# Optimization experiments

Hardware: AMD Instinct MI355X
Metric: run time of the kernel (lower is better)

## Reference

```python
import jax, jax.numpy as jnp
import numpy as np

D_MODEL = 1024
D_STATE = 32
EXPAND = 2
D_INNER = D_MODEL * EXPAND          # 2048
DT_RANK = D_MODEL // 16             # 64
LN_EPS = 1e-5


def setup_inputs() -> dict:
    key = jax.random.key(0)
    ks = jax.random.split(key, 9)
    s = 0.02
    x = jax.random.normal(ks[0], (2, 2048, D_MODEL), dtype=jnp.float32)
    W_in = jax.random.normal(ks[1], (2 * D_INNER, D_MODEL), dtype=jnp.float32) * s
    W_x = jax.random.normal(ks[2], (DT_RANK + 2 * D_STATE, D_INNER), dtype=jnp.float32) * s
    W_dt = jax.random.normal(ks[3], (D_INNER, DT_RANK), dtype=jnp.float32) * s
    b_dt = jax.random.normal(ks[4], (D_INNER,), dtype=jnp.float32) * s
    A_real0 = jax.random.normal(ks[5], (D_INNER, D_STATE), dtype=jnp.float32) * 0.5
    A_log_real = jnp.log(jnp.clip(-A_real0, 1e-4, None))
    A_imag = jax.random.normal(ks[6], (D_INNER, D_STATE), dtype=jnp.float32) * 0.1
    D_param = jnp.ones((D_INNER,), dtype=jnp.float32)
    W_out = jax.random.normal(ks[7], (D_MODEL, D_INNER), dtype=jnp.float32) * s
    ln_g = jnp.ones((D_MODEL,), dtype=jnp.float32)
    ln_b = jnp.zeros((D_MODEL,), dtype=jnp.float32)
    return {"x": x, "W_in": W_in, "W_x": W_x, "W_dt": W_dt, "b_dt": b_dt,
            "A_log_real": A_log_real, "A_imag": A_imag, "D_param": D_param,
            "W_out": W_out, "ln_g": ln_g, "ln_b": ln_b}


def _forward(x, W_in, W_x, W_dt, b_dt, A_log_real, A_imag, D_param, W_out, ln_g, ln_b):
    B, T, _ = x.shape
    residual = x
    # LayerNorm
    mu = jnp.mean(x, axis=-1, keepdims=True)
    var = jnp.mean((x - mu) ** 2, axis=-1, keepdims=True)
    xn = (x - mu) * jax.lax.rsqrt(var + LN_EPS) * ln_g + ln_b
    # in_proj -> (x_ssm, z)
    xz = jnp.einsum('btd,ed->bte', xn, W_in)            # (B,T,2*d_inner)
    x_ssm, z = jnp.split(xz, 2, axis=-1)
    # x_proj -> dt_low, B, C
    x_dbl = jnp.einsum('bte,re->btr', x_ssm, W_x)        # (B,T,dt_rank+2*d_state)
    dt_low = x_dbl[..., :DT_RANK]
    B_param = x_dbl[..., DT_RANK:DT_RANK + D_STATE]      # (B,T,N)
    C_param = x_dbl[..., DT_RANK + D_STATE:]             # (B,T,N)
    dt = jax.nn.softplus(jnp.einsum('btr,er->bte', dt_low, W_dt) + b_dt)  # (B,T,d_inner)
    # A = -exp(A_log_real) + i * A_imag, complex state split into (hr, hi)
    Ar = -jnp.exp(A_log_real)                             # (d_inner,N)
    Ai = A_imag

    def step(carry, inp):
        hr, hi = carry                                    # (B,d_inner,N)
        dt_t, B_t, C_t, x_t = inp                         # (B,d_inner),(B,N),(B,N),(B,d_inner)
        dtE = dt_t[:, :, None]                            # (B,d_inner,1)
        scale = jnp.exp(Ar[None] * dtE)
        ang = Ai[None] * dtE
        dAr = scale * jnp.cos(ang)
        dAi = scale * jnp.sin(ang)
        dBx = (dt_t * x_t)[:, :, None] * B_t[:, None, :]  # real input injection
        hr2 = dAr * hr - dAi * hi + dBx
        hi2 = dAr * hi + dAi * hr
        y = jnp.sum(hr2 * C_t[:, None, :], axis=-1)       # real part of (h * C).sum
        return (hr2, hi2), y

    h0 = jnp.zeros((B, D_INNER, D_STATE), dtype=x.dtype)
    xs = (jnp.transpose(dt, (1, 0, 2)), jnp.transpose(B_param, (1, 0, 2)),
          jnp.transpose(C_param, (1, 0, 2)), jnp.transpose(x_ssm, (1, 0, 2)))
    _, ys = jax.lax.scan(step, (h0, h0), xs)              # (T,B,d_inner)
    y = jnp.transpose(ys, (1, 0, 2)) + D_param * x_ssm
    y = y * jax.nn.silu(z)
    out = jnp.einsum('bte,de->btd', y, W_out)
    return residual + out  # dropout is identity at eval


def reference(x, W_in, W_x, W_dt, b_dt, A_log_real, A_imag, D_param, W_out, ln_g, ln_b):
    return _forward(x, W_in, W_x, W_dt, b_dt, A_log_real, A_imag, D_param, W_out, ln_g, ln_b)
```

## Files before the change

### kernel.cpp

```cpp
#include <hip/hip_runtime.h>
#include <math.h>

#define D_MODEL 1024
#define D_STATE 32
#define D_INNER 2048
#define DT_RANK 64
#define BT 4096
#define XZLD 4224
#define LN_EPS 1e-5f

typedef __attribute__((ext_vector_type(8))) short short8;
typedef __attribute__((ext_vector_type(4))) float f32x4;
typedef const __attribute__((address_space(1))) void* gp_t;
typedef __attribute__((address_space(3))) void* lp_t;

__device__ __forceinline__ ushort bf16r(float f) {
    unsigned u = __float_as_uint(f);
    u += 0x7fff + ((u >> 16) & 1);
    return (ushort)(u >> 16);
}

__device__ __forceinline__ float dpp_red16(float x) {
    int t;
    t = __builtin_amdgcn_update_dpp(0, __float_as_int(x), 0x111, 0xf, 0xf, true);
    x += __int_as_float(t);
    t = __builtin_amdgcn_update_dpp(0, __float_as_int(x), 0x112, 0xf, 0xf, true);
    x += __int_as_float(t);
    t = __builtin_amdgcn_update_dpp(0, __float_as_int(x), 0x114, 0xf, 0xf, true);
    x += __int_as_float(t);
    t = __builtin_amdgcn_update_dpp(0, __float_as_int(x), 0x118, 0xf, 0xf, true);
    x += __int_as_float(t);
    return x;
}

__global__ __launch_bounds__(256) void prep_weights(
    const float* __restrict__ W_in, const float* __restrict__ W_out,
    const float* __restrict__ W_dt, const float* __restrict__ W_x,
    ushort* __restrict__ Waug, ushort* __restrict__ Wout_bf,
    ushort* __restrict__ Wdt_bf, ushort* __restrict__ Wx_bf) {
    int bid = blockIdx.x;
    const float* src; ushort* dst; int i;
    if (bid < 4096)      { src = W_in;  dst = Waug;    i = bid * 256 + threadIdx.x; }
    else if (bid < 6144) { src = W_out; dst = Wout_bf; i = (bid - 4096) * 256 + threadIdx.x; }
    else if (bid < 6400) { src = W_x;   dst = Wx_bf;   i = (bid - 6144) * 256 + threadIdx.x; }
    else                 { src = W_dt;  dst = Wdt_bf;  i = (bid - 6400) * 256 + threadIdx.x; }
    float4 v = ((const float4*)src)[i];
    ushort4 o;
    o.x = bf16r(v.x); o.y = bf16r(v.y); o.z = bf16r(v.z); o.w = bf16r(v.w);
    ((ushort4*)dst)[i] = o;
}

__global__ __launch_bounds__(256) void cvt_dtlow(const float* __restrict__ xz,
                                                 ushort* __restrict__ out) {
    int i = blockIdx.x * 256 + threadIdx.x;
    int row = i >> 4, c = (i & 15) << 2;
    float4 v = *(const float4*)&xz[(size_t)row * XZLD + 4096 + c];
    ushort4 o;
    o.x = bf16r(v.x); o.y = bf16r(v.y); o.z = bf16r(v.z); o.w = bf16r(v.w);
    ((ushort4*)out)[i] = o;
}

__global__ __launch_bounds__(256) void transpose_cvt(const float* __restrict__ in,
                                                     ushort* __restrict__ out) {
    __shared__ float tile[32][33];
    int bx = blockIdx.x * 32;
    int by = blockIdx.y * 32;
    int tx = threadIdx.x & 31, ty = threadIdx.x >> 5;
    #pragma unroll
    for (int i = 0; i < 32; i += 8)
        tile[ty + i][tx] = in[(size_t)(bx + ty + i) * 1024 + by + tx];
    __syncthreads();
    #pragma unroll
    for (int i = 0; i < 32; i += 8)
        out[(size_t)(by + ty + i) * 2048 + bx + tx] = bf16r(tile[tx][ty + i]);
}

__global__ __launch_bounds__(256) void ln_kernel(const float* __restrict__ x,
                                                 const float* __restrict__ g,
                                                 const float* __restrict__ b,
                                                 ushort* __restrict__ xn) {
    int row = blockIdx.x;
    const float4* xr = (const float4*)(x + (size_t)row * D_MODEL);
    float4 v = xr[threadIdx.x];
    float s  = v.x + v.y + v.z + v.w;
    float ss = v.x*v.x + v.y*v.y + v.z*v.z + v.w*v.w;
    #pragma unroll
    for (int off = 32; off > 0; off >>= 1) {
        s  += __shfl_down(s,  off, 64);
        ss += __shfl_down(ss, off, 64);
    }
    __shared__ float rs[4], rss[4];
    int wave = threadIdx.x >> 6;
    if ((threadIdx.x & 63) == 0) { rs[wave] = s; rss[wave] = ss; }
    __syncthreads();
    s  = rs[0] + rs[1] + rs[2] + rs[3];
    ss = rss[0] + rss[1] + rss[2] + rss[3];
    float mu  = s * (1.f / D_MODEL);
    float var = ss * (1.f / D_MODEL) - mu * mu;
    float inv = rsqrtf(var + LN_EPS);
    float4 gv = ((const float4*)g)[threadIdx.x];
    float4 bv = ((const float4*)b)[threadIdx.x];
    ushort4 o;
    o.x = bf16r((v.x - mu) * inv * gv.x + bv.x);
    o.y = bf16r((v.y - mu) * inv * gv.y + bv.y);
    o.z = bf16r((v.z - mu) * inv * gv.z + bv.z);
    o.w = bf16r((v.w - mu) * inv * gv.w + bv.w);
    ((ushort4*)(xn + (size_t)row * D_MODEL))[threadIdx.x] = o;
}

template<int RESID, int ACT, int OBF>
__global__ __launch_bounds__(256) void gemm_bt_bf16(
    const ushort* __restrict__ A, const ushort* __restrict__ B,
    void* __restrict__ Cv, int ldc, int K,
    const float* __restrict__ resid, const float* __restrict__ bias)
{
    __shared__ __align__(16) ushort As[128 * 32];
    __shared__ __align__(16) ushort Bs[128 * 32];
    int tid = threadIdx.x;
    int bm = blockIdx.x * 128, bn = blockIdx.y * 128;
    int wave = tid >> 6, lane = tid & 63;
    int wm = (wave & 1) * 64, wn = (wave >> 1) * 64;
    int quad = lane >> 4, m16 = lane & 15;
    int grow = tid >> 2;
    int gcol = (tid & 3) * 8;
    const size_t a0 = (size_t)(bm + grow) * K + gcol;
    const size_t b0 = (size_t)(bn + grow) * K + gcol;
    char* asw = (char*)As + wave * 1024;
    char* bsw = (char*)Bs + wave * 1024;

    f32x4 acc[4][4] = {};
    for (int k0 = 0; k0 < K; k0 += 32) {
        __builtin_amdgcn_global_load_lds((gp_t)(A + a0 + k0),                 (lp_t)asw,          16, 0, 0);
        __builtin_amdgcn_global_load_lds((gp_t)(A + a0 + (size_t)64*K + k0),  (lp_t)(asw + 4096), 16, 0, 0);
        __builtin_amdgcn_global_load_lds((gp_t)(B + b0 + k0),                 (lp_t)bsw,          16, 0, 0);
        __builtin_amdgcn_global_load_lds((gp_t)(B + b0 + (size_t)64*K + k0),  (lp_t)(bsw + 4096), 16, 0, 0);
        __syncthreads();
        short8 af[4], bf[4];
        #pragma unroll
        for (int i = 0; i < 4; ++i)
            af[i] = *(const short8*)&As[(wm + i * 16 + m16) * 32 + quad * 8];
        #pragma unroll
        for (int j = 0; j < 4; ++j)
            bf[j] = *(const short8*)&Bs[(wn + j * 16 + m16) * 32 + quad * 8];
        #pragma unroll
        for (int i = 0; i < 4; ++i)
            #pragma unroll
            for (int j = 0; j < 4; ++j)
                acc[i][j] = __builtin_amdgcn_mfma_f32_16x16x32_bf16(
                    af[i], bf[j], acc[i][j], 0, 0, 0);
        __syncthreads();
    }
    #pragma unroll
    for (int i = 0; i < 4; ++i) {
        #pragma unroll
        for (int r = 0; r < 4; ++r) {
            int row = bm + wm + i * 16 + quad * 4 + r;
            #pragma unroll
            for (int j = 0; j < 4; ++j) {
                int col = bn + wn + j * 16 + m16;
                float v = acc[i][j][r];
                if (ACT == 1) {
                    v += bias[col];
                    v = (v > 20.f) ? v : __logf(1.f + __expf(v));
                }
                if (RESID) v += resid[(size_t)row * ldc + col];
                if (OBF) ((ushort*)Cv)[(size_t)row * ldc + col] = bf16r(v);
                else     ((float*) Cv)[(size_t)row * ldc + col] = v;
            }
        }
    }
}

__global__ __launch_bounds__(256) void scan_kernel(
    const float* __restrict__ xz,
    const float* __restrict__ dtm,
    const float* __restrict__ A_log_real,
    const float* __restrict__ A_imag,
    const float* __restrict__ D_param,
    ushort* __restrict__ y)
{
    const int tid  = threadIdx.x;
    const int lane = tid & 63;
    const int s    = tid & 31;
    const int elb  = tid >> 5;
    const int b    = blockIdx.x >> 8;
    const int e0   = (blockIdx.x & 255) << 3;
    const int e    = e0 + elb;
    const int stt  = tid >> 3, sk  = tid & 7;
    const int btp  = tid >> 4, bsp = tid & 15;
    const int q    = (lane >> 4) & 1;

    __shared__ __align__(16) float dxp[2][8][17][4];
    __shared__ __align__(16) float xzs[2][8][34][2];
    __shared__ __align__(16) float bcs[2][16][33][4];
    __shared__ __align__(16) float pp[8][2][32];

    const float Ar2  = -__expf(A_log_real[e * D_STATE + s]) * 1.44269504f;
    const float Ai2p = A_imag[e * D_STATE + s] * 0.15915494f;
    const float Dps  = D_param[e0 + sk];
    float hr = 0.f, hi = 0.f;
    const float* xzb = xz + (size_t)b * 2048 * XZLD;
    const float* bcb = xzb + 4096 + DT_RANK;
    const float* dtb = dtm + (size_t)b * 2048 * 2048;
    ushort*      yb  = y   + (size_t)b * 2048 * 2048;

    float r_d, r_x, r_z;
    float2 rB0, rC0, rB1, rC1;

#define LOADC(T0) do {                                                        \
    r_d = dtb[(size_t)((T0) + stt) * 2048 + e0 + sk];                         \
    r_x = xzb[(size_t)((T0) + stt) * XZLD + e0 + sk];                         \
    r_z = xzb[(size_t)((T0) + stt) * XZLD + 2048 + e0 + sk];                  \
    rB0 = *(const float2*)&bcb[(size_t)((T0) + 2*btp) * XZLD + 2*bsp];        \
    rC0 = *(const float2*)&bcb[(size_t)((T0) + 2*btp) * XZLD + 32 + 2*bsp];   \
    rB1 = *(const float2*)&bcb[(size_t)((T0) + 2*btp+1) * XZLD + 2*bsp];      \
    rC1 = *(const float2*)&bcb[(size_t)((T0) + 2*btp+1) * XZLD + 32 + 2*bsp]; \
  } while (0)

#define STAGE(NB) do {                                                        \
    float dtx = r_d * r_x;                                                    \
    float gg  = r_z / (1.f + __expf(-r_z));                                   \
    float Dx  = Dps * r_x;                                                    \
    *(float2*)&dxp[NB][sk][stt >> 1][(stt & 1) * 2] = make_float2(r_d, dtx);  \
    *(float2*)&xzs[NB][sk][stt] = make_float2(Dx, gg);                        \
    *(float4*)&bcs[NB][btp][2*bsp][0]   = make_float4(rB0.x, rC0.x, rB1.x, rC1.x); \
    *(float4*)&bcs[NB][btp][2*bsp+1][0] = make_float4(rB0.y, rC0.y, rB1.y, rC1.y); \
  } while (0)

    LOADC(0);
    STAGE(0);
    for (int c = 0; c < 64; ++c) {
        const int buf = c & 1;
        __syncthreads();
        if (c < 63) LOADC((c + 1) * 32);
        #pragma unroll
        for (int tp = 0; tp < 16; ++tp) {
            float4 dd = *(const float4*)&dxp[buf][elb][tp][0];
            float4 bc = *(const float4*)&bcs[buf][tp][s][0];
            float sc = __builtin_amdgcn_exp2f(Ar2 * dd.x);
            float u  = Ai2p * dd.x;
            float sa = __builtin_amdgcn_sinf(u), ca = __builtin_amdgcn_cosf(u);
            float dAr = sc * ca, dAi = sc * sa;
            float hrn = fmaf(dAr, hr, fmaf(-dAi, hi, dd.y * bc.x));
            hi = fmaf(dAr, hi, dAi * hr); hr = hrn;
            float p0 = hr * bc.y;
            sc = __builtin_amdgcn_exp2f(Ar2 * dd.z);
            u  = Ai2p * dd.z;
            sa = __builtin_amdgcn_sinf(u); ca = __builtin_amdgcn_cosf(u);
            dAr = sc * ca; dAi = sc * sa;
            hrn = fmaf(dAr, hr, fmaf(-dAi, hi, dd.w * bc.z));
            hi = fmaf(dAr, hi, dAi * hr); hr = hrn;
            float p1 = hr * bc.w;
            p0 = dpp_red16(p0);
            p1 = dpp_red16(p1);
            if ((lane & 15) == 15)
                *(float2*)&pp[elb][q][2 * tp] = make_float2(p0, p1);
        }
        float pA = pp[elb][0][s];
        float pB = pp[elb][1][s];
        float2 xg = *(const float2*)&xzs[buf][elb][s];
        yb[(size_t)(c * 32 + s) * 2048 + e] = bf16r((pA + pB + xg.x) * xg.y);
        if (c < 63) STAGE(buf ^ 1);
    }
#undef LOADC
#undef STAGE
}

extern "C" void kernel_launch(void* const* d_in, const int* in_sizes, int n_in,
                              void* d_out, int out_size, void* d_ws, size_t ws_size,
                              hipStream_t stream) {
    const float* x          = (const float*)d_in[0];
    const float* W_in       = (const float*)d_in[1];
    const float* W_x        = (const float*)d_in[2];
    const float* W_dt       = (const float*)d_in[3];
    const float* b_dt       = (const float*)d_in[4];
    const float* A_log_real = (const float*)d_in[5];
    const float* A_imag     = (const float*)d_in[6];
    const float* D_param    = (const float*)d_in[7];
    const float* W_out      = (const float*)d_in[8];
    const float* ln_g       = (const float*)d_in[9];
    const float* ln_b       = (const float*)d_in[10];
    float* out = (float*)d_out;

    char* ws = (char*)d_ws;
    float*  xz       = (float*) (ws);
    float*  dt       = (float*) (ws + ((size_t) 66 << 20));
    ushort* xn_bf    = (ushort*)(ws + ((size_t) 98 << 20));
    ushort* Waug     = (ushort*)(ws + ((size_t)106 << 20));
    ushort* y_bf     = (ushort*)(ws + ((size_t)115 << 20));
    ushort* Wout_bf  = (ushort*)(ws + ((size_t)131 << 20));
    ushort* Wdt_bf   = (ushort*)(ws + ((size_t)135 << 20));
    ushort* dtlow_bf = (ushort*)(ws + ((size_t)136 << 20));
    ushort* Wx_bf   = (ushort*)(ws + ((size_t)  1 << 20));
    ushort* WinT_bf = (ushort*)(ws + ((size_t)  2 << 20));

    prep_weights<<<6528, 256, 0, stream>>>(W_in, W_out, W_dt, W_x,
                                           Waug, Wout_bf, Wdt_bf, Wx_bf);
    transpose_cvt<<<dim3(64, 32), 256, 0, stream>>>(W_in, WinT_bf);
    gemm_bt_bf16<0,0,1><<<dim3(1, 8), 256, 0, stream>>>(
        Wx_bf, WinT_bf, Waug + (size_t)4096 * 1024, 1024, 2048, nullptr, nullptr);
    ln_kernel<<<BT, 256, 0, stream>>>(x, ln_g, ln_b, xn_bf);
    gemm_bt_bf16<0,0,0><<<dim3(BT/128, XZLD/128), 256, 0, stream>>>(
        xn_bf, Waug, xz, XZLD, D_MODEL, nullptr, nullptr);
    cvt_dtlow<<<256, 256, 0, stream>>>(xz, dtlow_bf);
    gemm_bt_bf16<0,1,0><<<dim3(BT/128, D_INNER/128), 256, 0, stream>>>(
        dtlow_bf, Wdt_bf, dt, D_INNER, DT_RANK, nullptr, b_dt);
    scan_kernel<<<512, 256, 0, stream>>>(xz, dt, A_log_real, A_imag, D_param, y_bf);
    gemm_bt_bf16<1,0,0><<<dim3(BT/128, D_MODEL/128), 256, 0, stream>>>(
        y_bf, Wout_bf, out, D_MODEL, D_INNER, x, nullptr);
}
```

Measured before the change: 501.7 us.

## Repack SSM intermediates into scan-friendly bf16 layouts and fuse epilogues

The in_proj GEMM epilogue now writes x and silu(z) as packed bf16 pairs in a per-channel-group, time-major layout, and writes dt_low and B/C as bf16 directly, which removes the fp32 xz buffer and the separate dt_low conversion kernel. The dt GEMM writes softplus output in the same grouped layout, so the scan reads contiguous per-group data. The scan stages y through a small LDS tile and stores it in a packed layout that a new N=64-tile out_proj GEMM reads directly. The weight transpose is merged into the prep kernel. This lowers memory traffic and launch count, at the cost of scattered epilogue stores and more bf16 rounding of x, z, B and C.

```diff
diff --git a/kernel.cpp b/kernel.cpp
--- a/kernel.cpp
+++ b/kernel.cpp
@@ -6,7 +6,6 @@
 #define D_INNER 2048
 #define DT_RANK 64
 #define BT 4096
-#define XZLD 4224
 #define LN_EPS 1e-5f
 
 typedef __attribute__((ext_vector_type(8))) short short8;
@@ -19,6 +18,8 @@
     u += 0x7fff + ((u >> 16) & 1);
     return (ushort)(u >> 16);
 }
+__device__ __forceinline__ float bflo(unsigned u) { return __uint_as_float(u << 16); }
+__device__ __forceinline__ float bfhi(unsigned u) { return __uint_as_float(u & 0xffff0000u); }
 
 __device__ __forceinline__ float dpp_red16(float x) {
     int t;
@@ -37,42 +38,33 @@
     const float* __restrict__ W_in, const float* __restrict__ W_out,
     const float* __restrict__ W_dt, const float* __restrict__ W_x,
     ushort* __restrict__ Waug, ushort* __restrict__ Wout_bf,
-    ushort* __restrict__ Wdt_bf, ushort* __restrict__ Wx_bf) {
+    ushort* __restrict__ Wdt_bf, ushort* __restrict__ Wx_bf,
+    ushort* __restrict__ WinT_bf) {
+    __shared__ float tile[32][33];
     int bid = blockIdx.x;
-    const float* src; ushort* dst; int i;
-    if (bid < 4096)      { src = W_in;  dst = Waug;    i = bid * 256 + threadIdx.x; }
-    else if (bid < 6144) { src = W_out; dst = Wout_bf; i = (bid - 4096) * 256 + threadIdx.x; }
-    else if (bid < 6400) { src = W_x;   dst = Wx_bf;   i = (bid - 6144) * 256 + threadIdx.x; }
-    else                 { src = W_dt;  dst = Wdt_bf;  i = (bid - 6400) * 256 + threadIdx.x; }
-    float4 v = ((const float4*)src)[i];
-    ushort4 o;
-    o.x = bf16r(v.x); o.y = bf16r(v.y); o.z = bf16r(v.z); o.w = bf16r(v.w);
-    ((ushort4*)dst)[i] = o;
-}
-
-__global__ __launch_bounds__(256) void cvt_dtlow(const float* __restrict__ xz,
-                                                 ushort* __restrict__ out) {
-    int i = blockIdx.x * 256 + threadIdx.x;
-    int row = i >> 4, c = (i & 15) << 2;
-    float4 v = *(const float4*)&xz[(size_t)row * XZLD + 4096 + c];
-    ushort4 o;
-    o.x = bf16r(v.x); o.y = bf16r(v.y); o.z = bf16r(v.z); o.w = bf16r(v.w);
-    ((ushort4*)out)[i] = o;
-}
-
-__global__ __launch_bounds__(256) void transpose_cvt(const float* __restrict__ in,
-                                                     ushort* __restrict__ out) {
-    __shared__ float tile[32][33];
-    int bx = blockIdx.x * 32;
-    int by = blockIdx.y * 32;
-    int tx = threadIdx.x & 31, ty = threadIdx.x >> 5;
-    #pragma unroll
-    for (int i = 0; i < 32; i += 8)
-        tile[ty + i][tx] = in[(size_t)(bx + ty + i) * 1024 + by + tx];
-    __syncthreads();
-    #pragma unroll
-    for (int i = 0; i < 32; i += 8)
-        out[(size_t)(by + ty + i) * 2048 + bx + tx] = bf16r(tile[tx][ty + i]);
+    if (bid < 6528) {
+        const float* src; ushort* dst; int i;
+        if (bid < 4096)      { src = W_in;  dst = Waug;    i = bid * 256 + threadIdx.x; }
+        else if (bid < 6144) { src = W_out; dst = Wout_bf; i = (bid - 4096) * 256 + threadIdx.x; }
+        else if (bid < 6400) { src = W_x;   dst = Wx_bf;   i = (bid - 6144) * 256 + threadIdx.x; }
+        else                 { src = W_dt;  dst = Wdt_bf;  i = (bid - 6400) * 256 + threadIdx.x; }
+        float4 v = ((const float4*)src)[i];
+        ushort4 o;
+        o.x = bf16r(v.x); o.y = bf16r(v.y); o.z = bf16r(v.z); o.w = bf16r(v.w);
+        ((ushort4*)dst)[i] = o;
+    } else {
+        int bid2 = bid - 6528;
+        int bx = (bid2 & 63) * 32;
+        int by = (bid2 >> 6) * 32;
+        int tx = threadIdx.x & 31, ty = threadIdx.x >> 5;
+        #pragma unroll
+        for (int i = 0; i < 32; i += 8)
+            tile[ty + i][tx] = W_in[(size_t)(bx + ty + i) * 1024 + by + tx];
+        __syncthreads();
+        #pragma unroll
+        for (int i = 0; i < 32; i += 8)
+            WinT_bf[(size_t)(by + ty + i) * 2048 + bx + tx] = bf16r(tile[tx][ty + i]);
+    }
 }
 
 __global__ __launch_bounds__(256) void ln_kernel(const float* __restrict__ x,
@@ -108,11 +100,13 @@
     ((ushort4*)(xn + (size_t)row * D_MODEL))[threadIdx.x] = o;
 }
 
-template<int RESID, int ACT, int OBF>
+template<int MODE>
 __global__ __launch_bounds__(256) void gemm_bt_bf16(
     const ushort* __restrict__ A, const ushort* __restrict__ B,
-    void* __restrict__ Cv, int ldc, int K,
-    const float* __restrict__ resid, const float* __restrict__ bias)
+    float* __restrict__ C, int ldc, int K,
+    const float* __restrict__ resid, const float* __restrict__ bias,
+    ushort* __restrict__ xg16, ushort* __restrict__ dtlow_bf,
+    ushort* __restrict__ bc_bf, float* __restrict__ dtp)
 {
     __shared__ __align__(16) ushort As[128 * 32];
     __shared__ __align__(16) ushort Bs[128 * 32];
@@ -159,33 +153,107 @@
             for (int j = 0; j < 4; ++j) {
                 int col = bn + wn + j * 16 + m16;
                 float v = acc[i][j][r];
-                if (ACT == 1) {
+                if (MODE == 0) {
+                    C[(size_t)row * ldc + col] = v;
+                } else if (MODE == 1) {
+                    ((ushort*)C)[(size_t)row * ldc + col] = bf16r(v);
+                } else if (MODE == 2) {
+                    int bb = row >> 11, t = row & 2047;
+                    if (col < 2048) {
+                        size_t slot = ((size_t)(bb * 256 + (col >> 3)) * 2048 + t) * 8 + (col & 7);
+                        xg16[slot * 2] = bf16r(v);
+                    } else if (col < 4096) {
+                        int e2 = col - 2048;
+                        float gg = v / (1.f + __expf(-v));
+                        size_t slot = ((size_t)(bb * 256 + (e2 >> 3)) * 2048 + t) * 8 + (e2 & 7);
+                        xg16[slot * 2 + 1] = bf16r(gg);
+                    } else if (col < 4160) {
+                        dtlow_bf[(size_t)row * 64 + (col - 4096)] = bf16r(v);
+                    } else {
+                        bc_bf[(size_t)row * 64 + (col - 4160)] = bf16r(v);
+                    }
+                } else {
                     v += bias[col];
                     v = (v > 20.f) ? v : __logf(1.f + __expf(v));
+                    int bb = row >> 11, t = row & 2047;
+                    dtp[((size_t)(bb * 256 + (col >> 3)) * 2048 + t) * 8 + (col & 7)] = v;
                 }
-                if (RESID) v += resid[(size_t)row * ldc + col];
-                if (OBF) ((ushort*)Cv)[(size_t)row * ldc + col] = bf16r(v);
-                else     ((float*) Cv)[(size_t)row * ldc + col] = v;
             }
         }
     }
 }
 
+__global__ __launch_bounds__(256) void gemm4_n64(
+    const ushort* __restrict__ A, const ushort* __restrict__ B,
+    float* __restrict__ C, const float* __restrict__ resid)
+{
+    __shared__ __align__(16) ushort As[128 * 32];
+    __shared__ __align__(16) ushort Bs[64 * 32];
+    int tid = threadIdx.x;
+    int bm = blockIdx.x * 128, bn = blockIdx.y * 64;
+    int wave = tid >> 6, lane = tid & 63;
+    int wm = (wave & 1) * 64, wn = (wave >> 1) * 32;
+    int quad = lane >> 4, m16 = lane & 15;
+    int grow = tid >> 2;
+    int gcol = (tid & 3) * 8;
+    int bb = bm >> 11, t0 = bm & 2047;
+    const size_t b0 = (size_t)(bn + grow) * 2048 + gcol;
+    char* asw = (char*)As + wave * 1024;
+    char* bsw = (char*)Bs + wave * 1024;
+
+    f32x4 acc[4][2] = {};
+    for (int k0 = 0; k0 < 2048; k0 += 32) {
+        size_t abase = (size_t)(bb * 256 + ((k0 + gcol) >> 3)) * 2048;
+        __builtin_amdgcn_global_load_lds((gp_t)(A + (abase + t0 + grow) * 8),      (lp_t)asw,          16, 0, 0);
+        __builtin_amdgcn_global_load_lds((gp_t)(A + (abase + t0 + grow + 64) * 8), (lp_t)(asw + 4096), 16, 0, 0);
+        __builtin_amdgcn_global_load_lds((gp_t)(B + b0 + k0),                      (lp_t)bsw,          16, 0, 0);
+        __syncthreads();
+        short8 af[4], bf[2];
+        #pragma unroll
+        for (int i = 0; i < 4; ++i)
+            af[i] = *(const short8*)&As[(wm + i * 16 + m16) * 32 + quad * 8];
+        #pragma unroll
+        for (int j = 0; j < 2; ++j)
+            bf[j] = *(const short8*)&Bs[(wn + j * 16 + m16) * 32 + quad * 8];
+        #pragma unroll
+        for (int i = 0; i < 4; ++i)
+            #pragma unroll
+            for (int j = 0; j < 2; ++j)
+                acc[i][j] = __builtin_amdgcn_mfma_f32_16x16x32_bf16(
+                    af[i], bf[j], acc[i][j], 0, 0, 0);
+        __syncthreads();
+    }
+    #pragma unroll
+    for (int i = 0; i < 4; ++i) {
+        #pragma unroll
+        for (int r = 0; r < 4; ++r) {
+            int row = bm + wm + i * 16 + quad * 4 + r;
+            #pragma unroll
+            for (int j = 0; j < 2; ++j) {
+                int col = bn + wn + j * 16 + m16;
+                C[(size_t)row * 1024 + col] =
+                    acc[i][j][r] + resid[(size_t)row * 1024 + col];
+            }
+        }
+    }
+}
+
 __global__ __launch_bounds__(256) void scan_kernel(
-    const float* __restrict__ xz,
-    const float* __restrict__ dtm,
+    const float* __restrict__ dtp,
+    const unsigned* __restrict__ xgp,
+    const ushort* __restrict__ bc_bf,
     const float* __restrict__ A_log_real,
     const float* __restrict__ A_imag,
     const float* __restrict__ D_param,
-    ushort* __restrict__ y)
+    unsigned* __restrict__ yq)
 {
     const int tid  = threadIdx.x;
     const int lane = tid & 63;
     const int s    = tid & 31;
     const int elb  = tid >> 5;
     const int b    = blockIdx.x >> 8;
-    const int e0   = (blockIdx.x & 255) << 3;
-    const int e    = e0 + elb;
+    const int eg   = blockIdx.x & 255;
+    const int e    = eg * 8 + elb;
     const int stt  = tid >> 3, sk  = tid & 7;
     const int btp  = tid >> 4, bsp = tid & 15;
     const int q    = (lane >> 4) & 1;
@@ -194,37 +262,32 @@
     __shared__ __align__(16) float xzs[2][8][34][2];
     __shared__ __align__(16) float bcs[2][16][33][4];
     __shared__ __align__(16) float pp[8][2][32];
+    __shared__ __align__(8)  ushort ytile[2][32][8];
 
     const float Ar2  = -__expf(A_log_real[e * D_STATE + s]) * 1.44269504f;
     const float Ai2p = A_imag[e * D_STATE + s] * 0.15915494f;
-    const float Dps  = D_param[e0 + sk];
+    const float Dps  = D_param[eg * 8 + sk];
     float hr = 0.f, hi = 0.f;
-    const float* xzb = xz + (size_t)b * 2048 * XZLD;
-    const float* bcb = xzb + 4096 + DT_RANK;
-    const float* dtb = dtm + (size_t)b * 2048 * 2048;
-    ushort*      yb  = y   + (size_t)b * 2048 * 2048;
-
-    float r_d, r_x, r_z;
-    float2 rB0, rC0, rB1, rC1;
-
-#define LOADC(T0) do {                                                        \
-    r_d = dtb[(size_t)((T0) + stt) * 2048 + e0 + sk];                         \
-    r_x = xzb[(size_t)((T0) + stt) * XZLD + e0 + sk];                         \
-    r_z = xzb[(size_t)((T0) + stt) * XZLD + 2048 + e0 + sk];                  \
-    rB0 = *(const float2*)&bcb[(size_t)((T0) + 2*btp) * XZLD + 2*bsp];        \
-    rC0 = *(const float2*)&bcb[(size_t)((T0) + 2*btp) * XZLD + 32 + 2*bsp];   \
-    rB1 = *(const float2*)&bcb[(size_t)((T0) + 2*btp+1) * XZLD + 2*bsp];      \
-    rC1 = *(const float2*)&bcb[(size_t)((T0) + 2*btp+1) * XZLD + 32 + 2*bsp]; \
+    const size_t dxbase = (size_t)(b * 256 + eg) * 2048;
+    const ushort* bcb = bc_bf + (size_t)b * 2048 * 64;
+
+    float r_d; unsigned r_xg, rB0, rC0, rB1, rC1;
+
+#define LOADC(T0) do {                                                          \
+    r_d  = dtp[(dxbase + (T0) + stt) * 8 + sk];                                 \
+    r_xg = xgp[(dxbase + (T0) + stt) * 8 + sk];                                 \
+    rB0 = *(const unsigned*)&bcb[(size_t)((T0) + 2*btp) * 64 + 2*bsp];          \
+    rC0 = *(const unsigned*)&bcb[(size_t)((T0) + 2*btp) * 64 + 32 + 2*bsp];     \
+    rB1 = *(const unsigned*)&bcb[(size_t)((T0) + 2*btp + 1) * 64 + 2*bsp];      \
+    rC1 = *(const unsigned*)&bcb[(size_t)((T0) + 2*btp + 1) * 64 + 32 + 2*bsp]; \
   } while (0)
 
-#define STAGE(NB) do {                                                        \
-    float dtx = r_d * r_x;                                                    \
-    float gg  = r_z / (1.f + __expf(-r_z));                                   \
-    float Dx  = Dps * r_x;                                                    \
-    *(float2*)&dxp[NB][sk][stt >> 1][(stt & 1) * 2] = make_float2(r_d, dtx);  \
-    *(float2*)&xzs[NB][sk][stt] = make_float2(Dx, gg);                        \
-    *(float4*)&bcs[NB][btp][2*bsp][0]   = make_float4(rB0.x, rC0.x, rB1.x, rC1.x); \
-    *(float4*)&bcs[NB][btp][2*bsp+1][0] = make_float4(rB0.y, rC0.y, rB1.y, rC1.y); \
+#define STAGE(NB) do {                                                          \
+    float xv = bflo(r_xg), gv = bfhi(r_xg);                                     \
+    *(float2*)&dxp[NB][sk][stt >> 1][(stt & 1) * 2] = make_float2(r_d, r_d * xv); \
+    *(float2*)&xzs[NB][sk][stt] = make_float2(Dps * xv, gv);                    \
+    *(float4*)&bcs[NB][btp][2*bsp][0]   = make_float4(bflo(rB0), bflo(rC0), bflo(rB1), bflo(rC1)); \
+    *(float4*)&bcs[NB][btp][2*bsp+1][0] = make_float4(bfhi(rB0), bfhi(rC0), bfhi(rB1), bfhi(rC1)); \
   } while (0)
 
     LOADC(0);
@@ -232,6 +295,11 @@
     for (int c = 0; c < 64; ++c) {
         const int buf = c & 1;
         __syncthreads();
+        if (c > 0 && tid < 128) {
+            int t = tid >> 2, qq = tid & 3;
+            unsigned v = *(const unsigned*)&ytile[buf ^ 1][t][(qq ^ (t & 3)) << 1];
+            yq[(dxbase + (size_t)(c - 1) * 32) * 4 + tid] = v;
+        }
         if (c < 63) LOADC((c + 1) * 32);
         #pragma unroll
         for (int tp = 0; tp < 16; ++tp) {
@@ -256,11 +324,20 @@
             if ((lane & 15) == 15)
                 *(float2*)&pp[elb][q][2 * tp] = make_float2(p0, p1);
         }
-        float pA = pp[elb][0][s];
-        float pB = pp[elb][1][s];
-        float2 xg = *(const float2*)&xzs[buf][elb][s];
-        yb[(size_t)(c * 32 + s) * 2048 + e] = bf16r((pA + pB + xg.x) * xg.y);
+        {
+            float pA = pp[elb][0][s];
+            float pB = pp[elb][1][s];
+            float2 xg2 = *(const float2*)&xzs[buf][elb][s];
+            ytile[buf][s][(((elb >> 1) ^ (s & 3)) << 1) | (elb & 1)] =
+                bf16r((pA + pB + xg2.x) * xg2.y);
+        }
         if (c < 63) STAGE(buf ^ 1);
+    }
+    __syncthreads();
+    if (tid < 128) {
+        int t = tid >> 2, qq = tid & 3;
+        unsigned v = *(const unsigned*)&ytile[1][t][(qq ^ (t & 3)) << 1];
+        yq[(dxbase + (size_t)63 * 32) * 4 + tid] = v;
     }
 #undef LOADC
 #undef STAGE
@@ -283,29 +360,33 @@
     float* out = (float*)d_out;
 
     char* ws = (char*)d_ws;
-    float*  xz       = (float*) (ws);
-    float*  dt       = (float*) (ws + ((size_t) 66 << 20));
-    ushort* xn_bf    = (ushort*)(ws + ((size_t) 98 << 20));
-    ushort* Waug     = (ushort*)(ws + ((size_t)106 << 20));
-    ushort* y_bf     = (ushort*)(ws + ((size_t)115 << 20));
-    ushort* Wout_bf  = (ushort*)(ws + ((size_t)131 << 20));
-    ushort* Wdt_bf   = (ushort*)(ws + ((size_t)135 << 20));
-    ushort* dtlow_bf = (ushort*)(ws + ((size_t)136 << 20));
-    ushort* Wx_bf   = (ushort*)(ws + ((size_t)  1 << 20));
-    ushort* WinT_bf = (ushort*)(ws + ((size_t)  2 << 20));
-
-    prep_weights<<<6528, 256, 0, stream>>>(W_in, W_out, W_dt, W_x,
-                                           Waug, Wout_bf, Wdt_bf, Wx_bf);
-    transpose_cvt<<<dim3(64, 32), 256, 0, stream>>>(W_in, WinT_bf);
-    gemm_bt_bf16<0,0,1><<<dim3(1, 8), 256, 0, stream>>>(
-        Wx_bf, WinT_bf, Waug + (size_t)4096 * 1024, 1024, 2048, nullptr, nullptr);
+    unsigned* xgp      = (unsigned*)(ws);
+    float*    dtp      = (float*)  (ws + ((size_t) 32 << 20));
+    ushort*   y_pk     = (ushort*) (ws + ((size_t) 64 << 20));
+    ushort*   dtlow_bf = (ushort*) (ws + ((size_t) 80 << 20));
+    ushort*   bc_bf    = (ushort*) (ws + ((size_t) 81 << 20));
+    ushort*   xn_bf    = (ushort*) (ws + ((size_t) 82 << 20));
+    ushort*   Waug     = (ushort*) (ws + ((size_t) 90 << 20));
+    ushort*   Wout_bf  = (ushort*) (ws + ((size_t) 99 << 20));
+    ushort*   Wdt_bf   = (ushort*) (ws + ((size_t)103 << 20));
+    ushort*   Wx_bf    = (ushort*) (ws + ((size_t)104 << 20));
+    ushort*   WinT_bf  = (ushort*) (ws + ((size_t)105 << 20));
+
+    prep_weights<<<8576, 256, 0, stream>>>(W_in, W_out, W_dt, W_x,
+                                           Waug, Wout_bf, Wdt_bf, Wx_bf, WinT_bf);
+    gemm_bt_bf16<1><<<dim3(1, 8), 256, 0, stream>>>(
+        Wx_bf, WinT_bf, (float*)(Waug + (size_t)4096 * 1024), 1024, 2048,
+        nullptr, nullptr, nullptr, nullptr, nullptr, nullptr);
     ln_kernel<<<BT, 256, 0, stream>>>(x, ln_g, ln_b, xn_bf);
-    gemm_bt_bf16<0,0,0><<<dim3(BT/128, XZLD/128), 256, 0, stream>>>(
-        xn_bf, Waug, xz, XZLD, D_MODEL, nullptr, nullptr);
-    cvt_dtlow<<<256, 256, 0, stream>>>(xz, dtlow_bf);
-    gemm_bt_bf16<0,1,0><<<dim3(BT/128, D_INNER/128), 256, 0, stream>>>(
-        dtlow_bf, Wdt_bf, dt, D_INNER, DT_RANK, nullptr, b_dt);
-    scan_kernel<<<512, 256, 0, stream>>>(xz, dt, A_log_real, A_imag, D_param, y_bf);
-    gemm_bt_bf16<1,0,0><<<dim3(BT/128, D_MODEL/128), 256, 0, stream>>>(
-        y_bf, Wout_bf, out, D_MODEL, D_INNER, x, nullptr);
-}
+    gemm_bt_bf16<2><<<dim3(BT/128, 33), 256, 0, stream>>>(
+        xn_bf, Waug, nullptr, 0, D_MODEL,
+        nullptr, nullptr, (ushort*)xgp, dtlow_bf, bc_bf, nullptr);
+    gemm_bt_bf16<3><<<dim3(BT/128, D_INNER/128), 256, 0, stream>>>(
+        dtlow_bf, Wdt_bf, nullptr, 0, DT_RANK,
+        nullptr, b_dt, nullptr, nullptr, nullptr, dtp);
+    scan_kernel<<<512, 256, 0, stream>>>(dtp, xgp, bc_bf,
+                                         A_log_real, A_imag, D_param,
+                                         (unsigned*)y_pk);
+    gemm4_n64<<<dim3(BT/128, D_MODEL/64), 256, 0, stream>>>(
+        y_pk, Wout_bf, out, x);
+}
```

New measurement: 497.5 us. About the same (-0.8%).
